# Kernel optimization log

Measured on AMD Instinct MI355X. Metric: run time of the kernel, lower is better.

## Reference

```python
import math
import jax, jax.numpy as jnp
import numpy as np

B, L, S, H, E, D = 2, 2048, 2048, 16, 64, 64

def setup_inputs() -> dict:
    key = jax.random.key(0)
    k1, k2, k3, k4, k5 = jax.random.split(key, 5)
    return {
        "queries": jax.random.normal(k1, (B, L, H, E), dtype=jnp.float32),
        "keys": jax.random.normal(k2, (B, S, H, E), dtype=jnp.float32),
        "values": jax.random.normal(k3, (B, S, H, D), dtype=jnp.float32),
        "tau": jax.random.uniform(k4, (B, 1), dtype=jnp.float32),
        "delta": jax.random.normal(k5, (B, S), dtype=jnp.float32),
        "attn_mask": jnp.zeros((1,), dtype=jnp.bool_),
    }

def reference(queries, keys, values, tau, delta, attn_mask):
    # queries: [B,L,H,E], keys: [B,S,H,E], values: [B,S,H,D]
    # tau: [B,1] -> [B,1,1,1]; delta: [B,S] -> [B,1,1,S]
    # mask_flag=False, so attn_mask is unused. Dropout is identity at eval.
    E_ = queries.shape[-1]
    scale = 1.0 / math.sqrt(E_)
    scores = jnp.einsum('blhe,bshe->bhls', queries, keys)  # [B,H,L,S]
    scores = scores * tau[:, None, None, :]                # de-stationary scale
    scores = scores + delta[:, None, None, :]              # de-stationary shift
    A = jax.nn.softmax(scale * scores, axis=-1)            # [B,H,L,S]
    V = jnp.einsum('bhls,bshd->blhd', A, values)           # [B,L,H,D]
    return V
```

## Files before the change

### kernel.cpp

```cpp
#include <hip/hip_runtime.h>


#define Bb 2
#define Ll 2048
#define Ss 2048
#define Hh 16
#define Ee 64
#define Dd 64
#define KV 64
#define NT 16

typedef _Float16 f16x8 __attribute__((ext_vector_type(8)));
typedef _Float16 f16x4 __attribute__((ext_vector_type(4)));
typedef __fp16 fp16x2 __attribute__((ext_vector_type(2)));
typedef float f32x4 __attribute__((ext_vector_type(4)));
typedef float f32x16 __attribute__((ext_vector_type(16)));

union Pk2 { fp16x2 h; unsigned u; };
union PackU { unsigned u[4]; f16x8 v; };

#define GLDS(gp, lp) __builtin_amdgcn_global_load_lds( \
    (const __attribute__((address_space(1))) void*)(gp), \
    (__attribute__((address_space(3))) void*)(lp), 16, 0, 0)

#if __has_builtin(__builtin_amdgcn_exp2f)
#define EXP2(x) __builtin_amdgcn_exp2f(x)
#else
#define EXP2(x) exp2f(x)
#endif

#define LOG2E 1.4426950408889634f

#define PSWAP(x, y) asm volatile("v_permlane32_swap_b32 %0, %1" : "+v"(x), "+v"(y))

__global__ __launch_bounds__(256)
void prepass_k(const float* __restrict__ K, _Float16* __restrict__ K16,
               const float* __restrict__ delta, float* __restrict__ delta2)
{
    const unsigned v = blockIdx.x * 256 + threadIdx.x;
    const unsigned e4 = v & 15;
    const unsigned h  = (v >> 4) & 15;
    const unsigned s  = (v >> 8) & (Ss - 1);
    const unsigned b  = v >> 19;
    const f32x4 src = ((const f32x4*)K)[v];
    f16x4 t;
    t[0] = (_Float16)src[0]; t[1] = (_Float16)src[1];
    t[2] = (_Float16)src[2]; t[3] = (_Float16)src[3];
    ((f16x4*)K16)[(((size_t)(b * Hh + h) * Ss + s) * 16) + e4] = t;
    if (v < (Bb * Ss) / 4) {
        const float sc = 0.125f * LOG2E;
        f32x4 dd = ((const f32x4*)delta)[v];
        ((f32x4*)delta2)[v] = (f32x4){sc * dd[0], sc * dd[1], sc * dd[2], sc * dd[3]};
    }
}

__global__ __launch_bounds__(256)
void prepass_v(const float* __restrict__ V, _Float16* __restrict__ VT16)
{
    __shared__ _Float16 TL[64][66];
    const int tid  = threadIdx.x;
    const int wave = tid >> 6;
    const int lane = tid & 63;
    const int bh = blockIdx.y;
    const int b  = bh >> 4;
    const int h  = bh & 15;
    const int s0 = blockIdx.x * 64;

    #pragma unroll
    for (int rr = 0; rr < 16; ++rr) {
        const int row = wave * 16 + rr;
        TL[row][lane] = (_Float16)V[((size_t)(b * Ss + s0 + row) * Hh + h) * Dd + lane];
    }
    __syncthreads();
    const int d  = tid >> 2;
    const int sq = (tid & 3) * 16;
    union { _Float16 h[16]; f16x8 v[2]; } tmp;
    #pragma unroll
    for (int i = 0; i < 16; ++i) tmp.h[i] = TL[sq + i][d];
    f16x8* dp = (f16x8*)(VT16 + ((size_t)(b * Hh + h) * Dd + d) * Ss + s0 + sq);
    dp[0] = tmp.v[0];
    dp[1] = tmp.v[1];
}


#define PBODY(T, CP, CN)                                                             \
{                                                                                    \
    const int sb_ = sBase + (T) * KV;                                                \
                                  \
    f32x4 dreg[2][4];                                                                \
    _Pragma("unroll")                                                                \
    for (int st = 0; st < 2; ++st)                                                   \
        _Pragma("unroll")                                                            \
        for (int q4 = 0; q4 < 4; ++q4)                                               \
            dreg[st][q4] = *(const f32x4*)(d2b + sb_ + st * 32 + q4 * 8 + hl * 4);   \
    if ((T) + 2 < NT) {                                                              \
        unsigned char* kw = stBase + ((T) & 1) * 8192 + wq * 1024;                   \
        GLDS(kb + (size_t)(sb_ + 2 * KV + row0) * 128 + slotS * 16, kw);             \
        GLDS(kb + (size_t)(sb_ + 2 * KV + row0 + 32) * 128 + slotS * 16, kw + 4096); \
    }                                                                                \
    if ((T) + 1 < NT) {                                                              \
        unsigned char* vw = stBase + 16384 + (((T) + 1) & 1) * 8192 + wq * 1024;     \
        GLDS(vtb + (size_t)row0 * (Ss * 2) + (sb_ + KV) * 2 + slotS * 16, vw);       \
        GLDS(vtb + (size_t)(row0 + 32) * (Ss * 2) + (sb_ + KV) * 2 + slotS * 16, vw + 4096); \
        const unsigned char* Ksm = stBase + (((T) + 1) & 1) * 8192;                  \
        _Pragma("unroll")                                                            \
        for (int st = 0; st < 2; ++st)                                               \
            _Pragma("unroll")                                                        \
            for (int i = 0; i < 16; ++i) CN[st][i] = 0.f;                            \
        __builtin_amdgcn_s_setprio(1);                                               \
        _Pragma("unroll")                                                            \
        for (int st = 0; st < 2; ++st) {                                             \
            const int krow = st * 32 + c31;                                          \
            _Pragma("unroll")                                                        \
            for (int es = 0; es < 4; ++es) {                                         \
                const int slot = (es * 2 + hl) ^ (krow & 7);                         \
                f16x8 ak = *(const f16x8*)(Ksm + krow * 128 + slot * 16);            \
                CN[st] = __builtin_amdgcn_mfma_f32_32x32x16_f16(ak, aq[es], CN[st], 0, 0, 0); \
            }                                                                        \
        }                                                                            \
        __builtin_amdgcn_s_setprio(0);                                               \
    }                                                                                \
    const unsigned char* Vsm = stBase + 16384 + ((T) & 1) * 8192;                    \
    _Pragma("unroll")                                                                \
    for (int st = 0; st < 2; ++st) {                                                 \
        float p[16];                                                                 \
        _Pragma("unroll")                                                            \
        for (int q4 = 0; q4 < 4; ++q4)                                               \
            _Pragma("unroll")                                                        \
            for (int j = 0; j < 4; ++j)                                              \
                p[q4 * 4 + j] = fmaf(alpha2, CP[st][q4 * 4 + j], dreg[st][q4][j]);   \
        float x0 = fmaxf(p[0], p[1]),  x1 = fmaxf(p[2], p[3]);                       \
        float x2 = fmaxf(p[4], p[5]),  x3 = fmaxf(p[6], p[7]);                       \
        float x4 = fmaxf(p[8], p[9]),  x5 = fmaxf(p[10], p[11]);                     \
        float x6 = fmaxf(p[12], p[13]), x7 = fmaxf(p[14], p[15]);                    \
        x0 = fmaxf(x0, x1); x2 = fmaxf(x2, x3); x4 = fmaxf(x4, x5); x6 = fmaxf(x6, x7); \
        const float tmax = fmaxf(fmaxf(x0, x2), fmaxf(x4, x6));                      \
        if (!__all(tmax <= m_run + 11.5416f)) {                                      \
            float rmax = fmaxf(tmax, __shfl_xor(tmax, 32));                          \
            const float m_new = fmaxf(m_run, rmax);                                  \
            const float corr = EXP2(m_run - m_new);                                  \
            l_run *= corr;                                                           \
            _Pragma("unroll")                                                        \
            for (int dt = 0; dt < 2; ++dt)                                           \
                _Pragma("unroll")                                                    \
                for (int i = 0; i < 16; ++i) osum[dt][i] *= corr;                    \
            m_run = m_new;                                                           \
        }                                                                            \
        _Pragma("unroll")                                                            \
        for (int i = 0; i < 16; ++i) p[i] = EXP2(p[i] - m_run);                      \
        {                                                                            \
            float s0 = p[0] + p[1],  s1 = p[2] + p[3];                               \
            float s2 = p[4] + p[5],  s3 = p[6] + p[7];                               \
            float s4 = p[8] + p[9],  s5 = p[10] + p[11];                             \
            float s6 = p[12] + p[13], s7 = p[14] + p[15];                            \
            s0 += s1; s2 += s3; s4 += s5; s6 += s7;                                  \
            l_run += (s0 + s2) + (s4 + s6);                                          \
        }                                                                            \
            \
        unsigned pk[8];                                                              \
        _Pragma("unroll")                                                            \
        for (int t4 = 0; t4 < 4; ++t4) {                                             \
            Pk2 u0, u1;                                                              \
            u0.h = __builtin_amdgcn_cvt_pkrtz(p[4 * t4], p[4 * t4 + 1]);             \
            u1.h = __builtin_amdgcn_cvt_pkrtz(p[4 * t4 + 2], p[4 * t4 + 3]);         \
            pk[t4 * 2] = u0.u;                                                       \
            pk[t4 * 2 + 1] = u1.u;                                                   \
        }                                                                            \
        __builtin_amdgcn_s_setprio(1);                                               \
        _Pragma("unroll")                                                            \
        for (int ks = 0; ks < 2; ++ks) {                                             \
            unsigned b0 = pk[ks * 4 + 0], b1 = pk[ks * 4 + 1];                       \
            unsigned b2 = pk[ks * 4 + 2], b3 = pk[ks * 4 + 3];                       \
            PSWAP(b0, b2);                                                           \
            PSWAP(b1, b3);                                                           \
            PackU bf;                                                                \
            bf.u[0] = b0; bf.u[1] = b1; bf.u[2] = b2; bf.u[3] = b3;                  \
            _Pragma("unroll")                                                        \
            for (int dt = 0; dt < 2; ++dt) {                                         \
                const int vrow = dt * 32 + c31;                                      \
                const int slot = (st * 4 + ks * 2 + hl) ^ (vrow & 7);                \
                f16x8 av = *(const f16x8*)(Vsm + vrow * 128 + slot * 16);            \
                osum[dt] = __builtin_amdgcn_mfma_f32_32x32x16_f16(av, bf.v, osum[dt], 0, 0, 0); \
            }                                                                        \
        }                                                                            \
        __builtin_amdgcn_s_setprio(0);                                               \
    }                                                                                \
    __syncthreads();                                                                 \
}

__global__ __launch_bounds__(512)
void dsattn_fwd_v10(const float* __restrict__ Q, const _Float16* __restrict__ K16,
                    const _Float16* __restrict__ VT16, const float* __restrict__ tau,
                    const float* __restrict__ delta2, float* __restrict__ out)
{
    extern __shared__ __align__(16) unsigned char smem[];

    const int tid  = threadIdx.x;
    const int wave = tid >> 6;
    const int halfId = wave >> 2;
    const int wq   = wave & 3;
    const int lane = tid & 63;
    const int c31  = lane & 31;
    const int hl   = lane >> 5;
    const int tid_h = tid & 255;

    const int bid = blockIdx.x;
    const int xcd = bid & 7;
    const int kk  = bid >> 3;
    const int bh  = xcd * 4 + (kk & 3);
    const int b   = bh >> 4;
    const int hd  = bh & 15;
    const int q0  = (kk >> 2) * 128;
    const int qw  = q0 + wq * 32;

    const float alpha2 = 0.125f * LOG2E * tau[b];

    f16x8 aq[4];
    {
        const float* qp = Q + (((size_t)b * Ll + qw + c31) * Hh + hd) * Ee;
        #pragma unroll
        for (int es = 0; es < 4; ++es) {
            const float* p = qp + es * 16 + hl * 8;
            f16x8 t;
            #pragma unroll
            for (int j = 0; j < 8; ++j) t[j] = (_Float16)p[j];
            aq[es] = t;
        }
    }

    f32x16 osum[2];
    #pragma unroll
    for (int dt = 0; dt < 2; ++dt)
        #pragma unroll
        for (int i = 0; i < 16; ++i) osum[dt][i] = 0.f;
    float m_run = -1e30f;
    float l_run = 0.0f;

    const unsigned char* kb  = (const unsigned char*)(K16 + (size_t)(b * Hh + hd) * Ss * Ee);
    const unsigned char* vtb = (const unsigned char*)(VT16 + (size_t)(b * Hh + hd) * Dd * Ss);
    const float* d2b = delta2 + (size_t)b * Ss;

    const int row0  = tid_h >> 3;
    const int slotS = (tid_h & 7) ^ (row0 & 7);
    unsigned char* stBase = smem + halfId * 32768;
    const int sBase = halfId * (Ss / 2);

    {
        unsigned char* kw0 = stBase + wq * 1024;
        GLDS(kb + (size_t)(sBase + row0) * 128 + slotS * 16, kw0);
        GLDS(kb + (size_t)(sBase + row0 + 32) * 128 + slotS * 16, kw0 + 4096);
        unsigned char* vw0 = stBase + 16384 + wq * 1024;
        GLDS(vtb + (size_t)row0 * (Ss * 2) + sBase * 2 + slotS * 16, vw0);
        GLDS(vtb + (size_t)(row0 + 32) * (Ss * 2) + sBase * 2 + slotS * 16, vw0 + 4096);
        unsigned char* kw1 = stBase + 8192 + wq * 1024;
        GLDS(kb + (size_t)(sBase + KV + row0) * 128 + slotS * 16, kw1);
        GLDS(kb + (size_t)(sBase + KV + row0 + 32) * 128 + slotS * 16, kw1 + 4096);
    }
    __syncthreads();

    f32x16 cA[2], cB[2];
    #pragma unroll
    for (int st = 0; st < 2; ++st)
        #pragma unroll
        for (int i = 0; i < 16; ++i) cA[st][i] = 0.f;
    {
        const unsigned char* Ksm = stBase;
        #pragma unroll
        for (int st = 0; st < 2; ++st) {
            const int krow = st * 32 + c31;
            #pragma unroll
            for (int es = 0; es < 4; ++es) {
                const int slot = (es * 2 + hl) ^ (krow & 7);
                f16x8 ak = *(const f16x8*)(Ksm + krow * 128 + slot * 16);
                cA[st] = __builtin_amdgcn_mfma_f32_32x32x16_f16(ak, aq[es], cA[st], 0, 0, 0);
            }
        }
    }
    __syncthreads();

    for (int t = 0; t < NT; t += 2) {
        PBODY(t,     cA, cB);
        PBODY(t + 1, cB, cA);
    }

    l_run += __shfl_xor(l_run, 32);

    float (*Part)[32][68] = (float (*)[32][68])smem;
    if (halfId == 1) {
        #pragma unroll
        for (int dt = 0; dt < 2; ++dt)
            #pragma unroll
            for (int q4 = 0; q4 < 4; ++q4) {
                f32x4 v = (f32x4){osum[dt][q4 * 4], osum[dt][q4 * 4 + 1],
                                  osum[dt][q4 * 4 + 2], osum[dt][q4 * 4 + 3]};
                *(f32x4*)&Part[wq][c31][dt * 32 + q4 * 8 + hl * 4] = v;
            }
        if (hl == 0) {
            Part[wq][c31][64] = m_run;
            Part[wq][c31][65] = l_run;
        }
    }
    __syncthreads();
    if (halfId == 0) {
        const float m1 = Part[wq][c31][64];
        const float l1 = Part[wq][c31][65];
        const float m  = fmaxf(m_run, m1);
        const float s0 = EXP2(m_run - m);
        const float s1 = EXP2(m1 - m);
        const float inv = 1.0f / (l_run * s0 + l1 * s1);
        #pragma unroll
        for (int dt = 0; dt < 2; ++dt)
            #pragma unroll
            for (int q4 = 0; q4 < 4; ++q4) {
                f32x4 p1 = *(const f32x4*)&Part[wq][c31][dt * 32 + q4 * 8 + hl * 4];
                #pragma unroll
                for (int j = 0; j < 4; ++j)
                    osum[dt][q4 * 4 + j] = (osum[dt][q4 * 4 + j] * s0 + p1[j] * s1) * inv;
            }
    }
    __syncthreads();
    float (*Osm)[68] = (float (*)[68])smem;
    if (halfId == 0) {
        #pragma unroll
        for (int dt = 0; dt < 2; ++dt)
            #pragma unroll
            for (int q4 = 0; q4 < 4; ++q4) {
                f32x4 v = (f32x4){osum[dt][q4 * 4], osum[dt][q4 * 4 + 1],
                                  osum[dt][q4 * 4 + 2], osum[dt][q4 * 4 + 3]};
                *(f32x4*)&Osm[wq * 32 + c31][dt * 32 + q4 * 8 + hl * 4] = v;
            }
    }
    __syncthreads();
    {
        float* ob = out + (((size_t)b * Ll + q0) * Hh + hd) * Dd;
        #pragma unroll
        for (int i = 0; i < 16; ++i) {
            const int r = wave * 16 + i;
            ob[(size_t)r * (Hh * Dd) + lane] = Osm[r][lane];
        }
    }
}

__global__ __launch_bounds__(256)
void dsattn_fwd(const float* __restrict__ Q, const float* __restrict__ K,
                const float* __restrict__ V, const float* __restrict__ tau,
                const float* __restrict__ delta, float* __restrict__ out)
{
    __shared__ __align__(16) unsigned char Ksm[32 * 128];
    __shared__ __align__(16) unsigned char VTsm[64 * 80];
    __shared__ float dsm[32];
    __shared__ float Osm[4][16][68];

    const int tid  = threadIdx.x;
    const int wave = tid >> 6;
    const int lane = tid & 63;
    const int lq   = lane & 15;
    const int g    = lane >> 4;

    const int bh = blockIdx.y;
    const int b  = bh >> 4;
    const int h  = bh & 15;
    const int q0 = blockIdx.x * 64;

    const float alpha = 0.125f * tau[b];

    f16x8 aq[2];
    {
        const float* qp = Q + (((long)b * Ll + q0 + wave * 16 + lq) * Hh + h) * Ee;
        #pragma unroll
        for (int es = 0; es < 2; ++es) {
            const float* p = qp + es * 32 + g * 8;
            f16x8 t;
            #pragma unroll
            for (int j = 0; j < 8; ++j) t[j] = (_Float16)p[j];
            aq[es] = t;
        }
    }

    f32x4 osum[4];
    #pragma unroll
    for (int i = 0; i < 4; ++i) osum[i] = (f32x4){0.f, 0.f, 0.f, 0.f};
    float m_run = -1e30f, l_run = 0.0f;

    const float* kb = K + ((long)b * Ss * Hh + h) * Ee;
    const float* vb = V + ((long)b * Ss * Hh + h) * Dd;
    const float* db = delta + (long)b * Ss;

    const int kr    = tid >> 3;
    const int kc    = (tid & 7) * 8;
    const int kslot = (((tid & 7) ^ (kr & 7)) * 16);
    const int vd    = tid & 63;
    const int vsh   = tid >> 6;

    for (int sb = 0; sb < Ss; sb += 32) {
        __syncthreads();
        {
            const float* src = kb + (long)(sb + kr) * (Hh * Ee) + kc;
            f16x8 t;
            #pragma unroll
            for (int j = 0; j < 8; ++j) t[j] = (_Float16)src[j];
            *(f16x8*)(Ksm + kr * 128 + kslot) = t;
        }
        {
            const float* src = vb + (long)(sb + vsh * 8) * (Hh * Dd) + vd;
            f16x8 t;
            #pragma unroll
            for (int j = 0; j < 8; ++j) t[j] = (_Float16)src[j * (Hh * Dd)];
            *(f16x8*)(VTsm + vd * 80 + vsh * 16) = t;
        }
        if (tid < 32) dsm[tid] = 0.125f * db[sb + tid];
        __syncthreads();

        float p[8];
        float tmax = -1e30f;
        #pragma unroll
        for (int t = 0; t < 2; ++t) {
            f32x4 c = (f32x4){0.f, 0.f, 0.f, 0.f};
            #pragma unroll
            for (int es = 0; es < 2; ++es) {
                const int srow = t * 16 + lq;
                const int slot = ((es * 4 + g) ^ (srow & 7)) * 16;
                f16x8 ak = *(const f16x8*)(Ksm + srow * 128 + slot);
                c = __builtin_amdgcn_mfma_f32_16x16x32_f16(ak, aq[es], c, 0, 0, 0);
            }
            #pragma unroll
            for (int j = 0; j < 4; ++j) {
                float z = alpha * c[j] + dsm[t * 16 + 4 * g + j];
                p[t * 4 + j] = z;
                tmax = fmaxf(tmax, z);
            }
        }
        tmax = fmaxf(tmax, __shfl_xor(tmax, 16));
        tmax = fmaxf(tmax, __shfl_xor(tmax, 32));
        const float m_new = fmaxf(m_run, tmax);
        const float corr  = __expf(m_run - m_new);
        float psum = 0.f;
        #pragma unroll
        for (int i = 0; i < 8; ++i) { p[i] = __expf(p[i] - m_new); psum += p[i]; }
        psum += __shfl_xor(psum, 16);
        psum += __shfl_xor(psum, 32);
        l_run = l_run * corr + psum;
        m_run = m_new;
        #pragma unroll
        for (int dt = 0; dt < 4; ++dt)
            #pragma unroll
            for (int j = 0; j < 4; ++j)
                osum[dt][j] *= corr;

        Pk2 u00, u01, u10, u11;
        u00.h = __builtin_amdgcn_cvt_pkrtz(p[0], p[1]);
        u01.h = __builtin_amdgcn_cvt_pkrtz(p[2], p[3]);
        u10.h = __builtin_amdgcn_cvt_pkrtz(p[4], p[5]);
        u11.h = __builtin_amdgcn_cvt_pkrtz(p[6], p[7]);
        const int srcA = lq + 32 * (g & 1);
        const int srcB = srcA + 16;
        unsigned a00 = __shfl(u00.u, srcA), a01 = __shfl(u01.u, srcA);
        unsigned a10 = __shfl(u10.u, srcA), a11 = __shfl(u11.u, srcA);
        unsigned b00 = __shfl(u00.u, srcB), b01 = __shfl(u01.u, srcB);
        unsigned b10 = __shfl(u10.u, srcB), b11 = __shfl(u11.u, srcB);
        const bool hi = (g >= 2);
        PackU bp;
        bp.u[0] = hi ? a10 : a00;
        bp.u[1] = hi ? a11 : a01;
        bp.u[2] = hi ? b10 : b00;
        bp.u[3] = hi ? b11 : b01;

        #pragma unroll
        for (int dt = 0; dt < 4; ++dt) {
            f16x8 av = *(const f16x8*)(VTsm + (dt * 16 + lq) * 80 + g * 16);
            osum[dt] = __builtin_amdgcn_mfma_f32_16x16x32_f16(av, bp.v, osum[dt], 0, 0, 0);
        }
    }

    const float inv = 1.0f / l_run;
    #pragma unroll
    for (int dt = 0; dt < 4; ++dt)
        #pragma unroll
        for (int j = 0; j < 4; ++j)
            Osm[wave][lq][dt * 16 + 4 * g + j] = osum[dt][j] * inv;
    __syncthreads();
    {
        float* ob = out + (((long)b * Ll + q0 + wave * 16) * Hh + h) * Dd;
        #pragma unroll
        for (int r = 0; r < 16; ++r)
            ob[(long)r * (Hh * Dd) + lane] = Osm[wave][r][lane];
    }
}

extern "C" void kernel_launch(void* const* d_in, const int* in_sizes, int n_in,
                              void* d_out, int out_size, void* d_ws, size_t ws_size,
                              hipStream_t stream) {
    const float* Q     = (const float*)d_in[0];
    const float* K     = (const float*)d_in[1];
    const float* V     = (const float*)d_in[2];
    const float* tau   = (const float*)d_in[3];
    const float* delta = (const float*)d_in[4];
    float* out = (float*)d_out;

    const size_t elems = (size_t)Bb * Hh * Ss * Ee;
    const size_t need  = elems * 2 * 2 + (size_t)Bb * Ss * 4;

    if (ws_size >= need) {
        _Float16* K16    = (_Float16*)d_ws;
        _Float16* VT16   = K16 + elems;
        float*    delta2 = (float*)(VT16 + elems);
        hipLaunchKernelGGL(prepass_k, dim3(elems / 4 / 256), dim3(256), 0, stream,
                           K, K16, delta, delta2);
        hipLaunchKernelGGL(prepass_v, dim3(Ss / 64, Bb * Hh), dim3(256), 0, stream, V, VT16);
        hipLaunchKernelGGL(dsattn_fwd_v10, dim3(512), dim3(512), 65536, stream,
                           Q, K16, VT16, tau, delta2, out);
    } else {
        hipLaunchKernelGGL(dsattn_fwd, dim3(Ll / 64, Bb * Hh), dim3(256), 0, stream,
                           Q, K, V, tau, delta, out);
    }
}
```

Measured before the change: 81.35 us.

## Load K and V fragments directly from global memory instead of LDS staging

Result: slower. 152.9 us (+87.9%).

```diff
diff --git a/kernel.cpp b/kernel.cpp
--- a/kernel.cpp
+++ b/kernel.cpp
@@ -18,10 +18,6 @@
 
 union Pk2 { fp16x2 h; unsigned u; };
 union PackU { unsigned u[4]; f16x8 v; };
-
-#define GLDS(gp, lp) __builtin_amdgcn_global_load_lds( \
-    (const __attribute__((address_space(1))) void*)(gp), \
-    (__attribute__((address_space(3))) void*)(lp), 16, 0, 0)
 
 #if __has_builtin(__builtin_amdgcn_exp2f)
 #define EXP2(x) __builtin_amdgcn_exp2f(x)
@@ -82,114 +78,8 @@
     dp[1] = tmp.v[1];
 }
 
-
-#define PBODY(T, CP, CN)                                                             \
-{                                                                                    \
-    const int sb_ = sBase + (T) * KV;                                                \
-                                  \
-    f32x4 dreg[2][4];                                                                \
-    _Pragma("unroll")                                                                \
-    for (int st = 0; st < 2; ++st)                                                   \
-        _Pragma("unroll")                                                            \
-        for (int q4 = 0; q4 < 4; ++q4)                                               \
-            dreg[st][q4] = *(const f32x4*)(d2b + sb_ + st * 32 + q4 * 8 + hl * 4);   \
-    if ((T) + 2 < NT) {                                                              \
-        unsigned char* kw = stBase + ((T) & 1) * 8192 + wq * 1024;                   \
-        GLDS(kb + (size_t)(sb_ + 2 * KV + row0) * 128 + slotS * 16, kw);             \
-        GLDS(kb + (size_t)(sb_ + 2 * KV + row0 + 32) * 128 + slotS * 16, kw + 4096); \
-    }                                                                                \
-    if ((T) + 1 < NT) {                                                              \
-        unsigned char* vw = stBase + 16384 + (((T) + 1) & 1) * 8192 + wq * 1024;     \
-        GLDS(vtb + (size_t)row0 * (Ss * 2) + (sb_ + KV) * 2 + slotS * 16, vw);       \
-        GLDS(vtb + (size_t)(row0 + 32) * (Ss * 2) + (sb_ + KV) * 2 + slotS * 16, vw + 4096); \
-        const unsigned char* Ksm = stBase + (((T) + 1) & 1) * 8192;                  \
-        _Pragma("unroll")                                                            \
-        for (int st = 0; st < 2; ++st)                                               \
-            _Pragma("unroll")                                                        \
-            for (int i = 0; i < 16; ++i) CN[st][i] = 0.f;                            \
-        __builtin_amdgcn_s_setprio(1);                                               \
-        _Pragma("unroll")                                                            \
-        for (int st = 0; st < 2; ++st) {                                             \
-            const int krow = st * 32 + c31;                                          \
-            _Pragma("unroll")                                                        \
-            for (int es = 0; es < 4; ++es) {                                         \
-                const int slot = (es * 2 + hl) ^ (krow & 7);                         \
-                f16x8 ak = *(const f16x8*)(Ksm + krow * 128 + slot * 16);            \
-                CN[st] = __builtin_amdgcn_mfma_f32_32x32x16_f16(ak, aq[es], CN[st], 0, 0, 0); \
-            }                                                                        \
-        }                                                                            \
-        __builtin_amdgcn_s_setprio(0);                                               \
-    }                                                                                \
-    const unsigned char* Vsm = stBase + 16384 + ((T) & 1) * 8192;                    \
-    _Pragma("unroll")                                                                \
-    for (int st = 0; st < 2; ++st) {                                                 \
-        float p[16];                                                                 \
-        _Pragma("unroll")                                                            \
-        for (int q4 = 0; q4 < 4; ++q4)                                               \
-            _Pragma("unroll")                                                        \
-            for (int j = 0; j < 4; ++j)                                              \
-                p[q4 * 4 + j] = fmaf(alpha2, CP[st][q4 * 4 + j], dreg[st][q4][j]);   \
-        float x0 = fmaxf(p[0], p[1]),  x1 = fmaxf(p[2], p[3]);                       \
-        float x2 = fmaxf(p[4], p[5]),  x3 = fmaxf(p[6], p[7]);                       \
-        float x4 = fmaxf(p[8], p[9]),  x5 = fmaxf(p[10], p[11]);                     \
-        float x6 = fmaxf(p[12], p[13]), x7 = fmaxf(p[14], p[15]);                    \
-        x0 = fmaxf(x0, x1); x2 = fmaxf(x2, x3); x4 = fmaxf(x4, x5); x6 = fmaxf(x6, x7); \
-        const float tmax = fmaxf(fmaxf(x0, x2), fmaxf(x4, x6));                      \
-        if (!__all(tmax <= m_run + 11.5416f)) {                                      \
-            float rmax = fmaxf(tmax, __shfl_xor(tmax, 32));                          \
-            const float m_new = fmaxf(m_run, rmax);                                  \
-            const float corr = EXP2(m_run - m_new);                                  \
-            l_run *= corr;                                                           \
-            _Pragma("unroll")                                                        \
-            for (int dt = 0; dt < 2; ++dt)                                           \
-                _Pragma("unroll")                                                    \
-                for (int i = 0; i < 16; ++i) osum[dt][i] *= corr;                    \
-            m_run = m_new;                                                           \
-        }                                                                            \
-        _Pragma("unroll")                                                            \
-        for (int i = 0; i < 16; ++i) p[i] = EXP2(p[i] - m_run);                      \
-        {                                                                            \
-            float s0 = p[0] + p[1],  s1 = p[2] + p[3];                               \
-            float s2 = p[4] + p[5],  s3 = p[6] + p[7];                               \
-            float s4 = p[8] + p[9],  s5 = p[10] + p[11];                             \
-            float s6 = p[12] + p[13], s7 = p[14] + p[15];                            \
-            s0 += s1; s2 += s3; s4 += s5; s6 += s7;                                  \
-            l_run += (s0 + s2) + (s4 + s6);                                          \
-        }                                                                            \
-            \
-        unsigned pk[8];                                                              \
-        _Pragma("unroll")                                                            \
-        for (int t4 = 0; t4 < 4; ++t4) {                                             \
-            Pk2 u0, u1;                                                              \
-            u0.h = __builtin_amdgcn_cvt_pkrtz(p[4 * t4], p[4 * t4 + 1]);             \
-            u1.h = __builtin_amdgcn_cvt_pkrtz(p[4 * t4 + 2], p[4 * t4 + 3]);         \
-            pk[t4 * 2] = u0.u;                                                       \
-            pk[t4 * 2 + 1] = u1.u;                                                   \
-        }                                                                            \
-        __builtin_amdgcn_s_setprio(1);                                               \
-        _Pragma("unroll")                                                            \
-        for (int ks = 0; ks < 2; ++ks) {                                             \
-            unsigned b0 = pk[ks * 4 + 0], b1 = pk[ks * 4 + 1];                       \
-            unsigned b2 = pk[ks * 4 + 2], b3 = pk[ks * 4 + 3];                       \
-            PSWAP(b0, b2);                                                           \
-            PSWAP(b1, b3);                                                           \
-            PackU bf;                                                                \
-            bf.u[0] = b0; bf.u[1] = b1; bf.u[2] = b2; bf.u[3] = b3;                  \
-            _Pragma("unroll")                                                        \
-            for (int dt = 0; dt < 2; ++dt) {                                         \
-                const int vrow = dt * 32 + c31;                                      \
-                const int slot = (st * 4 + ks * 2 + hl) ^ (vrow & 7);                \
-                f16x8 av = *(const f16x8*)(Vsm + vrow * 128 + slot * 16);            \
-                osum[dt] = __builtin_amdgcn_mfma_f32_32x32x16_f16(av, bf.v, osum[dt], 0, 0, 0); \
-            }                                                                        \
-        }                                                                            \
-        __builtin_amdgcn_s_setprio(0);                                               \
-    }                                                                                \
-    __syncthreads();                                                                 \
-}
-
-__global__ __launch_bounds__(512)
-void dsattn_fwd_v10(const float* __restrict__ Q, const _Float16* __restrict__ K16,
+__global__ __launch_bounds__(512, 4)
+void dsattn_fwd_v11(const float* __restrict__ Q, const _Float16* __restrict__ K16,
                     const _Float16* __restrict__ VT16, const float* __restrict__ tau,
                     const float* __restrict__ delta2, float* __restrict__ out)
 {
@@ -202,7 +92,6 @@
     const int lane = tid & 63;
     const int c31  = lane & 31;
     const int hl   = lane >> 5;
-    const int tid_h = tid & 255;
 
     const int bid = blockIdx.x;
     const int xcd = bid & 7;
@@ -236,51 +125,93 @@
     float m_run = -1e30f;
     float l_run = 0.0f;
 
-    const unsigned char* kb  = (const unsigned char*)(K16 + (size_t)(b * Hh + hd) * Ss * Ee);
-    const unsigned char* vtb = (const unsigned char*)(VT16 + (size_t)(b * Hh + hd) * Dd * Ss);
+    const _Float16* kbh = K16 + (size_t)(b * Hh + hd) * Ss * Ee;
+    const _Float16* vbh = VT16 + (size_t)(b * Hh + hd) * Dd * Ss;
     const float* d2b = delta2 + (size_t)b * Ss;
-
-    const int row0  = tid_h >> 3;
-    const int slotS = (tid_h & 7) ^ (row0 & 7);
-    unsigned char* stBase = smem + halfId * 32768;
     const int sBase = halfId * (Ss / 2);
 
-    {
-        unsigned char* kw0 = stBase + wq * 1024;
-        GLDS(kb + (size_t)(sBase + row0) * 128 + slotS * 16, kw0);
-        GLDS(kb + (size_t)(sBase + row0 + 32) * 128 + slotS * 16, kw0 + 4096);
-        unsigned char* vw0 = stBase + 16384 + wq * 1024;
-        GLDS(vtb + (size_t)row0 * (Ss * 2) + sBase * 2 + slotS * 16, vw0);
-        GLDS(vtb + (size_t)(row0 + 32) * (Ss * 2) + sBase * 2 + slotS * 16, vw0 + 4096);
-        unsigned char* kw1 = stBase + 8192 + wq * 1024;
-        GLDS(kb + (size_t)(sBase + KV + row0) * 128 + slotS * 16, kw1);
-        GLDS(kb + (size_t)(sBase + KV + row0 + 32) * 128 + slotS * 16, kw1 + 4096);
-    }
-    __syncthreads();
-
-    f32x16 cA[2], cB[2];
-    #pragma unroll
-    for (int st = 0; st < 2; ++st)
-        #pragma unroll
-        for (int i = 0; i < 16; ++i) cA[st][i] = 0.f;
-    {
-        const unsigned char* Ksm = stBase;
+    for (int t = 0; t < NT; ++t) {
+        const int sb = sBase + t * KV;
         #pragma unroll
         for (int st = 0; st < 2; ++st) {
-            const int krow = st * 32 + c31;
+            const _Float16* kp = kbh + (size_t)(sb + st * 32 + c31) * Ee + hl * 8;
+            f32x16 c;
+            #pragma unroll
+            for (int i = 0; i < 16; ++i) c[i] = 0.f;
+            __builtin_amdgcn_s_setprio(1);
             #pragma unroll
             for (int es = 0; es < 4; ++es) {
-                const int slot = (es * 2 + hl) ^ (krow & 7);
-                f16x8 ak = *(const f16x8*)(Ksm + krow * 128 + slot * 16);
-                cA[st] = __builtin_amdgcn_mfma_f32_32x32x16_f16(ak, aq[es], cA[st], 0, 0, 0);
-            }
-        }
-    }
-    __syncthreads();
-
-    for (int t = 0; t < NT; t += 2) {
-        PBODY(t,     cA, cB);
-        PBODY(t + 1, cB, cA);
+                f16x8 kv = *(const f16x8*)(kp + es * 16);
+                c = __builtin_amdgcn_mfma_f32_32x32x16_f16(kv, aq[es], c, 0, 0, 0);
+            }
+            __builtin_amdgcn_s_setprio(0);
+
+            f32x4 dreg[4];
+            #pragma unroll
+            for (int q4 = 0; q4 < 4; ++q4)
+                dreg[q4] = *(const f32x4*)(d2b + sb + st * 32 + q4 * 8 + hl * 4);
+            float p[16];
+            #pragma unroll
+            for (int q4 = 0; q4 < 4; ++q4)
+                #pragma unroll
+                for (int j = 0; j < 4; ++j)
+                    p[q4 * 4 + j] = fmaf(alpha2, c[q4 * 4 + j], dreg[q4][j]);
+            float x0 = fmaxf(p[0], p[1]),  x1 = fmaxf(p[2], p[3]);
+            float x2 = fmaxf(p[4], p[5]),  x3 = fmaxf(p[6], p[7]);
+            float x4 = fmaxf(p[8], p[9]),  x5 = fmaxf(p[10], p[11]);
+            float x6 = fmaxf(p[12], p[13]), x7 = fmaxf(p[14], p[15]);
+            x0 = fmaxf(x0, x1); x2 = fmaxf(x2, x3); x4 = fmaxf(x4, x5); x6 = fmaxf(x6, x7);
+            const float tmax = fmaxf(fmaxf(x0, x2), fmaxf(x4, x6));
+            if (!__all(tmax <= m_run + 11.5416f)) {
+                float rmax = fmaxf(tmax, __shfl_xor(tmax, 32));
+                const float m_new = fmaxf(m_run, rmax);
+                const float corr = EXP2(m_run - m_new);
+                l_run *= corr;
+                #pragma unroll
+                for (int dt = 0; dt < 2; ++dt)
+                    #pragma unroll
+                    for (int i = 0; i < 16; ++i) osum[dt][i] *= corr;
+                m_run = m_new;
+            }
+            #pragma unroll
+            for (int i = 0; i < 16; ++i) p[i] = EXP2(p[i] - m_run);
+            {
+                float s0 = p[0] + p[1],  s1 = p[2] + p[3];
+                float s2 = p[4] + p[5],  s3 = p[6] + p[7];
+                float s4 = p[8] + p[9],  s5 = p[10] + p[11];
+                float s6 = p[12] + p[13], s7 = p[14] + p[15];
+                s0 += s1; s2 += s3; s4 += s5; s6 += s7;
+                l_run += (s0 + s2) + (s4 + s6);
+            }
+
+            unsigned pk[8];
+            #pragma unroll
+            for (int t4 = 0; t4 < 4; ++t4) {
+                Pk2 u0, u1;
+                u0.h = __builtin_amdgcn_cvt_pkrtz(p[4 * t4], p[4 * t4 + 1]);
+                u1.h = __builtin_amdgcn_cvt_pkrtz(p[4 * t4 + 2], p[4 * t4 + 3]);
+                pk[t4 * 2] = u0.u;
+                pk[t4 * 2 + 1] = u1.u;
+            }
+            __builtin_amdgcn_s_setprio(1);
+            #pragma unroll
+            for (int ks = 0; ks < 2; ++ks) {
+                unsigned b0 = pk[ks * 4 + 0], b1 = pk[ks * 4 + 1];
+                unsigned b2 = pk[ks * 4 + 2], b3 = pk[ks * 4 + 3];
+                PSWAP(b0, b2);
+                PSWAP(b1, b3);
+                PackU bf;
+                bf.u[0] = b0; bf.u[1] = b1; bf.u[2] = b2; bf.u[3] = b3;
+                #pragma unroll
+                for (int dt = 0; dt < 2; ++dt) {
+                    const _Float16* vp = vbh + (size_t)(dt * 32 + c31) * Ss
+                                         + sb + st * 32 + ks * 16 + hl * 8;
+                    f16x8 vv = *(const f16x8*)vp;
+                    osum[dt] = __builtin_amdgcn_mfma_f32_32x32x16_f16(vv, bf.v, osum[dt], 0, 0, 0);
+                }
+            }
+            __builtin_amdgcn_s_setprio(0);
+        }
     }
 
     l_run += __shfl_xor(l_run, 32);
@@ -507,7 +438,7 @@
         hipLaunchKernelGGL(prepass_k, dim3(elems / 4 / 256), dim3(256), 0, stream,
                            K, K16, delta, delta2);
         hipLaunchKernelGGL(prepass_v, dim3(Ss / 64, Bb * Hh), dim3(256), 0, stream, V, VT16);
-        hipLaunchKernelGGL(dsattn_fwd_v10, dim3(512), dim3(512), 65536, stream,
+        hipLaunchKernelGGL(dsattn_fwd_v11, dim3(512), dim3(512), 34816, stream,
                            Q, K16, VT16, tau, delta2, out);
     } else {
         hipLaunchKernelGGL(dsattn_fwd, dim3(Ll / 64, Bb * Hh), dim3(256), 0, stream,
```
